# Kernel optimization log

Measured on AMD Instinct MI355X. Metric: run time of the kernel, lower is better.

The kernel has to match this reference:

```python
import jax, jax.numpy as jnp
import numpy as np

N_NODES = 100000
NEG_SLOPE = 0.01


def setup_inputs() -> dict:
    key = jax.random.key(0)
    k1, k2, k3, k4 = jax.random.split(key, 4)
    E = 1600000
    x = jax.random.normal(k1, (N_NODES, 256), dtype=jnp.float32)
    edge_index = jax.random.randint(k2, (2, E), 0, N_NODES, dtype=jnp.int64)
    # Glorot-ish init for GCN linear weights
    W1 = jax.random.normal(k3, (256, 128), dtype=jnp.float32) / np.sqrt(256.0)
    b1 = jnp.zeros((128,), dtype=jnp.float32)
    W2 = jax.random.normal(k4, (128, 64), dtype=jnp.float32) / np.sqrt(128.0)
    b2 = jnp.zeros((64,), dtype=jnp.float32)
    return {"x": x, "edge_index": edge_index, "W1": W1, "b1": b1, "W2": W2, "b2": b2}


def _gcn_norm(edge_index, n_nodes):
    # Add self-loops (PyG GCNConv default), symmetric normalization.
    loops = jnp.arange(n_nodes, dtype=edge_index.dtype)
    src = jnp.concatenate([edge_index[0], loops])
    dst = jnp.concatenate([edge_index[1], loops])
    deg = jax.ops.segment_sum(jnp.ones_like(dst, dtype=jnp.float32), dst,
                              num_segments=n_nodes)
    dinv = jnp.where(deg > 0, 1.0 / jnp.sqrt(deg), 0.0)
    norm = dinv[src] * dinv[dst]  # [E + N]
    return src, dst, norm


def _gcn_conv(h, W, b, src, dst, norm, n_nodes):
    h = h @ W                              # [N, out] linear transform first
    msg = h[src] * norm[:, None]           # gather + edge weighting
    agg = jax.ops.segment_sum(msg, dst, num_segments=n_nodes)  # scatter-add
    return agg + b


def reference(x, edge_index, W1, b1, W2, b2):
    n = x.shape[0]
    src, dst, norm = _gcn_norm(edge_index, n)
    h = _gcn_conv(x, W1, b1, src, dst, norm, n)
    h = jnp.where(h >= 0, h, NEG_SLOPE * h)  # leaky_relu, slope 0.01
    return _gcn_conv(h, W2, b2, src, dst, norm, n)
```

## Files before the change

### kernel.cpp

```cpp
#include <hip/hip_runtime.h>
#include <hip/hip_bf16.h>
#include <stdint.h>

#define GPART 512
#define BSHIFT 9
#define BSIZE 512
#define MAXNB 512

typedef short short8 __attribute__((ext_vector_type(8)));
typedef float f32x4 __attribute__((ext_vector_type(4)));
union U4S8 { uint4 u; short8 s; };

static __device__ __forceinline__ float bflo(uint32_t h){ return __uint_as_float(h << 16); }
static __device__ __forceinline__ float bfhi(uint32_t h){ return __uint_as_float(h & 0xFFFF0000u); }
static __device__ __forceinline__ uint32_t f2bf_bits(float f){
  uint32_t u = __float_as_uint(f);
  return (u + 0x7FFFu + ((u >> 16) & 1u)) >> 16;
}
static __device__ __forceinline__ uint32_t pack2bf(float lo, float hi){
  return f2bf_bits(lo) | (f2bf_bits(hi) << 16);
}

__global__ __launch_bounds__(256) void k_hist(const int* __restrict__ dst, int E, int NB,
    int* __restrict__ gHist){
  __shared__ int lh[MAXNB];
  int blk = blockIdx.x;
  for (int i = threadIdx.x; i < NB; i += 256) lh[i] = 0;
  __syncthreads();
  int chunk = (E + GPART - 1) / GPART;
  int e0 = blk * chunk, e1 = min(E, e0 + chunk);
  for (int e = e0 + threadIdx.x; e < e1; e += 256)
    atomicAdd(&lh[dst[e] >> BSHIFT], 1);
  __syncthreads();
  for (int i = threadIdx.x; i < NB; i += 256) gHist[i * GPART + blk] = lh[i];
}

__global__ __launch_bounds__(64) void k_scanA(int* __restrict__ gHist,
    int* __restrict__ bucketTotal){
  int b = blockIdx.x;
  int lane = threadIdx.x;
  int carry = 0;
  #pragma unroll
  for (int r = 0; r < GPART/64; ++r){
    int v = gHist[b*GPART + r*64 + lane];
    int pref = v;
    #pragma unroll
    for (int off = 1; off < 64; off <<= 1){ int t = __shfl_up(pref, off); if (lane >= off) pref += t; }
    int tot = __shfl(pref, 63);
    gHist[b*GPART + r*64 + lane] = carry + pref - v;
    carry += tot;
  }
  if (lane == 0) bucketTotal[b] = carry;
}

__global__ __launch_bounds__(64) void k_scanB(const int* __restrict__ bucketTotal, int NB,
    int* __restrict__ bucketBase){
  int lane = threadIdx.x;
  int carry = 0;
  for (int r = 0; r*64 < NB; ++r){
    int idx = r*64 + lane;
    int v = (idx < NB) ? bucketTotal[idx] : 0;
    int pref = v;
    #pragma unroll
    for (int off = 1; off < 64; off <<= 1){ int t = __shfl_up(pref, off); if (lane >= off) pref += t; }
    int tot = __shfl(pref, 63);
    if (idx < NB) bucketBase[idx] = carry + pref - v;
    carry += tot;
  }
}

__global__ __launch_bounds__(256) void k_scatter(const int* __restrict__ src,
    const int* __restrict__ dst, int E, int NB,
    const int* __restrict__ gHist, const int* __restrict__ bucketBase,
    uint32_t* __restrict__ edgesP){
  __shared__ int lpos[MAXNB];
  int blk = blockIdx.x;
  for (int i = threadIdx.x; i < NB; i += 256) lpos[i] = 0;
  __syncthreads();
  int chunk = (E + GPART - 1) / GPART;
  int e0 = blk * chunk, e1 = min(E, e0 + chunk);
  for (int e = e0 + threadIdx.x; e < e1; e += 256){
    int s = src[e], d = dst[e];
    int b = d >> BSHIFT;
    int o = atomicAdd(&lpos[b], 1);
    int pos = bucketBase[b] + gHist[b*GPART + blk] + o;
    edgesP[pos] = (uint32_t)s | ((uint32_t)(d & (BSIZE-1)) << 23);
  }
}

__global__ __launch_bounds__(256) void k_buildcsr(const uint32_t* __restrict__ edgesP,
    const int* __restrict__ bucketBase, const int* __restrict__ bucketTotal,
    int n, int* __restrict__ start, int* __restrict__ cnt, float* __restrict__ dinv,
    int* __restrict__ csr){
  __shared__ int cnt_l[BSIZE], start_l[BSIZE], fp[BSIZE];
  int b = blockIdx.x;
  int base = bucketBase[b], total = bucketTotal[b];
  int d0 = b << BSHIFT;
  int tid = threadIdx.x;
  for (int i = tid; i < BSIZE; i += 256){ cnt_l[i] = 0; fp[i] = 0; }
  __syncthreads();
  for (int i = tid; i < total; i += 256)
    atomicAdd(&cnt_l[edgesP[base + i] >> 23], 1);
  __syncthreads();
  if (tid < 64){
    int lane = tid, carry = 0;
    #pragma unroll
    for (int r = 0; r < BSIZE/64; ++r){
      int v = cnt_l[r*64 + lane];
      int pref = v;
      #pragma unroll
      for (int off = 1; off < 64; off <<= 1){ int t = __shfl_up(pref, off); if (lane >= off) pref += t; }
      int tot = __shfl(pref, 63);
      start_l[r*64 + lane] = carry + pref - v;
      carry += tot;
    }
  }
  __syncthreads();
  for (int i = tid; i < BSIZE; i += 256){
    int d = d0 + i;
    if (d < n){
      int c = cnt_l[i];
      cnt[d] = c;
      start[d] = base + start_l[i];
      dinv[d] = rsqrtf((float)(c + 1));
    }
  }
  for (int i = tid; i < total; i += 256){
    uint32_t w = edgesP[base + i];
    int dl = (int)(w >> 23);
    int s = (int)(w & 0x7FFFFFu);
    int p = atomicAdd(&fp[dl], 1);
    csr[base + start_l[dl] + p] = s;
  }
}

__global__ __launch_bounds__(256) void k_packW(const float* __restrict__ W,
    uint4* __restrict__ Wf, int K, int Nc){
  int s = blockIdx.x * 256 + threadIdx.x;
  int total = (K >> 5) * (Nc >> 4) * 64;
  if (s >= total) return;
  int lane = s & 63;
  int frag = s >> 6;
  int NT = Nc >> 4;
  int nt = frag % NT, ks = frag / NT;
  int col = nt*16 + (lane & 15);
  int k0  = ks*32 + (lane >> 4)*8;
  float v[8];
  #pragma unroll
  for (int e = 0; e < 8; ++e) v[e] = W[(size_t)(k0 + e)*Nc + col];
  uint4 u;
  u.x = pack2bf(v[0], v[1]); u.y = pack2bf(v[2], v[3]);
  u.z = pack2bf(v[4], v[5]); u.w = pack2bf(v[6], v[7]);
  Wf[s] = u;
}

__global__ __launch_bounds__(256) void k_gemm1_mfma(const float* __restrict__ X,
    const uint4* __restrict__ W1f, unsigned short* __restrict__ H1, int n){
  int wv = (int)((blockIdx.x * 256u + threadIdx.x) >> 6);
  int lane = threadIdx.x & 63;
  int row0 = wv * 16;
  if (row0 >= n) return;
  int rA = lane & 15, kg = lane >> 4;
  f32x4 acc[8];
  #pragma unroll
  for (int nt = 0; nt < 8; ++nt) acc[nt] = (f32x4){0.f, 0.f, 0.f, 0.f};
  int r0 = min(row0 + rA, n - 1);
  const float* x0 = X + (size_t)r0*256 + kg*8;
  float4 fa = *(const float4*)(x0);
  float4 fb = *(const float4*)(x0 + 4);
  for (int ks = 0; ks < 8; ++ks){
    U4S8 a;
    a.u.x = pack2bf(fa.x, fa.y); a.u.y = pack2bf(fa.z, fa.w);
    a.u.z = pack2bf(fb.x, fb.y); a.u.w = pack2bf(fb.z, fb.w);
    if (ks < 7){
      fa = *(const float4*)(x0 + (ks+1)*32);
      fb = *(const float4*)(x0 + (ks+1)*32 + 4);
    }
    #pragma unroll
    for (int nt = 0; nt < 8; ++nt){
      U4S8 b; b.u = W1f[(ks*8 + nt)*64 + lane];
      acc[nt] = __builtin_amdgcn_mfma_f32_16x16x32_bf16(a.s, b.s, acc[nt], 0, 0, 0);
    }
  }
  #pragma unroll
  for (int r = 0; r < 4; ++r){
    int row = row0 + kg*4 + r;
    if (row < n){
      #pragma unroll
      for (int nt = 0; nt < 8; ++nt)
        H1[(size_t)row*128 + nt*16 + rA] = (unsigned short)f2bf_bits(acc[nt][r]);
    }
  }
}

__global__ __launch_bounds__(256) void k_agg1(const uint32_t* __restrict__ H1,
    const int* __restrict__ csr,
    const int* __restrict__ start, const int* __restrict__ cnt,
    const float* __restrict__ dinv, const float* __restrict__ b1,
    uint32_t* __restrict__ A1, int n){
  int w = (int)((blockIdx.x * blockDim.x + threadIdx.x) >> 6);
  int lane = threadIdx.x & 63;
  if (w >= n) return;
  float dw = dinv[w];
  uint32_t h = H1[(size_t)w*64 + lane];
  float sw = dw * dw;
  float a0 = sw * bflo(h), a1 = sw * bfhi(h);
  int e0 = start[w], deg = cnt[w];
  for (int base = 0; base < deg; base += 64){
    int nin = min(64, deg - base);
    int sE = (lane < nin) ? csr[e0 + base + lane] : 0;
    float dvE = (lane < nin) ? dinv[sE] : 0.f;
    for (int j = 0; j < nin; j += 8){
      int ss[8]; float wts[8];
      #pragma unroll
      for (int u = 0; u < 8; ++u){
        int jj = j + u;
        int s = __shfl(sE, jj & 63);
        float dv = __shfl(dvE, jj & 63);
        bool ok = jj < nin;
        ss[u] = ok ? s : w;
        wts[u] = ok ? dv * dw : 0.f;
      }
      uint32_t hh[8];
      #pragma unroll
      for (int u = 0; u < 8; ++u) hh[u] = H1[(size_t)ss[u]*64 + lane];
      #pragma unroll
      for (int u = 0; u < 8; ++u){
        a0 = fmaf(wts[u], bflo(hh[u]), a0);
        a1 = fmaf(wts[u], bfhi(hh[u]), a1);
      }
    }
  }
  a0 += b1[lane*2]; a1 += b1[lane*2+1];
  a0 = (a0 >= 0.f) ? a0 : 0.01f * a0;
  a1 = (a1 >= 0.f) ? a1 : 0.01f * a1;
  A1[(size_t)w*64 + lane] = pack2bf(a0, a1);
}

__global__ __launch_bounds__(256) void k_gemm2_mfma(const uint4* __restrict__ A1,
    const uint4* __restrict__ W2f, unsigned short* __restrict__ H2, int n){
  int wv = (int)((blockIdx.x * 256u + threadIdx.x) >> 6);
  int lane = threadIdx.x & 63;
  int row0 = wv * 16;
  if (row0 >= n) return;
  int rA = lane & 15, kg = lane >> 4;
  f32x4 acc[4];
  #pragma unroll
  for (int nt = 0; nt < 4; ++nt) acc[nt] = (f32x4){0.f, 0.f, 0.f, 0.f};
  int r0 = min(row0 + rA, n - 1);
  const uint4* arow = A1 + (size_t)r0*16 + kg;
  uint4 u = arow[0];
  #pragma unroll
  for (int ks = 0; ks < 4; ++ks){
    U4S8 a; a.u = u;
    if (ks < 3) u = arow[(ks+1)*4];
    #pragma unroll
    for (int nt = 0; nt < 4; ++nt){
      U4S8 b; b.u = W2f[(ks*4 + nt)*64 + lane];
      acc[nt] = __builtin_amdgcn_mfma_f32_16x16x32_bf16(a.s, b.s, acc[nt], 0, 0, 0);
    }
  }
  #pragma unroll
  for (int r = 0; r < 4; ++r){
    int row = row0 + kg*4 + r;
    if (row < n){
      #pragma unroll
      for (int nt = 0; nt < 4; ++nt)
        H2[(size_t)row*64 + nt*16 + rA] = (unsigned short)f2bf_bits(acc[nt][r]);
    }
  }
}

__global__ __launch_bounds__(256) void k_agg2(const unsigned short* __restrict__ H2,
    const int* __restrict__ csr,
    const int* __restrict__ start, const int* __restrict__ cnt,
    const float* __restrict__ dinv, const float* __restrict__ b2,
    float* __restrict__ out, int n){
  int w = (int)((blockIdx.x * blockDim.x + threadIdx.x) >> 6);
  int lane = threadIdx.x & 63;
  if (w >= n) return;
  float dw = dinv[w];
  float a = dw * dw * __uint_as_float(((uint32_t)H2[(size_t)w*64 + lane]) << 16);
  int e0 = start[w], deg = cnt[w];
  for (int base = 0; base < deg; base += 64){
    int nin = min(64, deg - base);
    int sE = (lane < nin) ? csr[e0 + base + lane] : 0;
    float dvE = (lane < nin) ? dinv[sE] : 0.f;
    for (int j = 0; j < nin; j += 8){
      int ss[8]; float wts[8];
      #pragma unroll
      for (int u = 0; u < 8; ++u){
        int jj = j + u;
        int s = __shfl(sE, jj & 63);
        float dv = __shfl(dvE, jj & 63);
        bool ok = jj < nin;
        ss[u] = ok ? s : w;
        wts[u] = ok ? dv * dw : 0.f;
      }
      unsigned short hh[8];
      #pragma unroll
      for (int u = 0; u < 8; ++u) hh[u] = H2[(size_t)ss[u]*64 + lane];
      #pragma unroll
      for (int u = 0; u < 8; ++u)
        a = fmaf(wts[u], __uint_as_float(((uint32_t)hh[u]) << 16), a);
    }
  }
  out[(size_t)w*64 + lane] = a + b2[lane];
}

extern "C" void kernel_launch(void* const* d_in, const int* in_sizes, int n_in,
                              void* d_out, int out_size, void* d_ws, size_t ws_size,
                              hipStream_t stream){
  const float* x  = (const float*)d_in[0];
  const int*   ei = (const int*)d_in[1];
  const float* W1 = (const float*)d_in[2];
  const float* b1 = (const float*)d_in[3];
  const float* W2 = (const float*)d_in[4];
  const float* b2 = (const float*)d_in[5];
  float* out = (float*)d_out;

  int N = in_sizes[0] / 256;
  int E = in_sizes[1] / 2;
  int NB = (N + BSIZE - 1) >> BSHIFT;

  char* p = (char*)d_ws;
  uint32_t* H1   = (uint32_t*)p;  p += (size_t)N*64*4;
  uint32_t* A1   = (uint32_t*)p;  p += (size_t)N*64*4;
  uint32_t* H2   = (uint32_t*)p;  p += (size_t)N*32*4;
  uint32_t* edgesP=(uint32_t*)p;  p += (size_t)E*4;
  int* csr       = (int*)p;       p += (size_t)E*4;
  int* gHist     = (int*)p;       p += (size_t)NB*GPART*4;
  int* bucketTotal=(int*)p;       p += (size_t)((NB+63)&~63)*4;
  int* bucketBase= (int*)p;       p += (size_t)((NB+63)&~63)*4;
  uint4* W1f     = (uint4*)p;     p += 8*8*64*16;
  uint4* W2f     = (uint4*)p;     p += 4*4*64*16;
  int* start     = (int*)p;       p += (size_t)N*4;
  int* cnt       = (int*)p;       p += (size_t)N*4;
  float* dinv    = (float*)p;     p += (size_t)N*4;

  const int* srcIdx = ei;
  const int* dstIdx = ei + E;

  int nW = (N + 15) / 16;
  int nWaveBlocks = (nW + 3) / 4;

  k_packW<<<(8*8*64 + 255)/256, 256, 0, stream>>>(W1, W1f, 256, 128);
  k_packW<<<(4*4*64 + 255)/256, 256, 0, stream>>>(W2, W2f, 128, 64);
  k_hist<<<GPART, 256, 0, stream>>>(dstIdx, E, NB, gHist);
  k_scanA<<<NB, 64, 0, stream>>>(gHist, bucketTotal);
  k_scanB<<<1, 64, 0, stream>>>(bucketTotal, NB, bucketBase);
  k_scatter<<<GPART, 256, 0, stream>>>(srcIdx, dstIdx, E, NB, gHist, bucketBase, edgesP);
  k_buildcsr<<<NB, 256, 0, stream>>>(edgesP, bucketBase, bucketTotal, N, start, cnt, dinv, csr);
  k_gemm1_mfma<<<nWaveBlocks, 256, 0, stream>>>(x, W1f, (unsigned short*)H1, N);
  k_agg1<<<(N+3)/4, 256, 0, stream>>>(H1, csr, start, cnt, dinv, b1, A1, N);
  k_gemm2_mfma<<<nWaveBlocks, 256, 0, stream>>>((const uint4*)A1, W2f, (unsigned short*)H2, N);
  k_agg2<<<(N+3)/4, 256, 0, stream>>>((const unsigned short*)H2, csr, start, cnt, dinv, b2, out, N);
}
```

Baseline: 214.0 us.

## Precompute edge weights into CSR and vectorize aggregation gathers across edge groups

CSR construction is split into two kernels, so the second can store each neighbour index together with its precomputed normalization weight as an int2. This removes the dependent dinv[src] gather from both aggregation kernels. The aggregation kernels now read feature rows as 16-byte vectors, with sub-groups of the wave handling different edges at once, then combine partial sums with cross-lane xor shuffles. The cost is twice the CSR storage and traffic, one extra kernel launch, and a shuffle reduction at the end of each aggregation.

```diff
diff --git a/kernel.cpp b/kernel.cpp
--- a/kernel.cpp
+++ b/kernel.cpp
@@ -88,16 +88,15 @@
   }
 }
 
-__global__ __launch_bounds__(256) void k_buildcsr(const uint32_t* __restrict__ edgesP,
+__global__ __launch_bounds__(256) void k_csr_p1(const uint32_t* __restrict__ edgesP,
     const int* __restrict__ bucketBase, const int* __restrict__ bucketTotal,
-    int n, int* __restrict__ start, int* __restrict__ cnt, float* __restrict__ dinv,
-    int* __restrict__ csr){
-  __shared__ int cnt_l[BSIZE], start_l[BSIZE], fp[BSIZE];
+    int n, int* __restrict__ start, int* __restrict__ cnt, float* __restrict__ dinv){
+  __shared__ int cnt_l[BSIZE], start_l[BSIZE];
   int b = blockIdx.x;
   int base = bucketBase[b], total = bucketTotal[b];
   int d0 = b << BSHIFT;
   int tid = threadIdx.x;
-  for (int i = tid; i < BSIZE; i += 256){ cnt_l[i] = 0; fp[i] = 0; }
+  for (int i = tid; i < BSIZE; i += 256) cnt_l[i] = 0;
   __syncthreads();
   for (int i = tid; i < total; i += 256)
     atomicAdd(&cnt_l[edgesP[base + i] >> 23], 1);
@@ -125,12 +124,26 @@
       dinv[d] = rsqrtf((float)(c + 1));
     }
   }
+}
+
+__global__ __launch_bounds__(256) void k_csr_p2(const uint32_t* __restrict__ edgesP,
+    const int* __restrict__ bucketBase, const int* __restrict__ bucketTotal,
+    const int* __restrict__ start, const float* __restrict__ dinv,
+    int2* __restrict__ csr){
+  __shared__ int fp[BSIZE];
+  int b = blockIdx.x;
+  int base = bucketBase[b], total = bucketTotal[b];
+  int d0 = b << BSHIFT;
+  int tid = threadIdx.x;
+  for (int i = tid; i < BSIZE; i += 256) fp[i] = 0;
+  __syncthreads();
   for (int i = tid; i < total; i += 256){
     uint32_t w = edgesP[base + i];
     int dl = (int)(w >> 23);
     int s = (int)(w & 0x7FFFFFu);
     int p = atomicAdd(&fp[dl], 1);
-    csr[base + start_l[dl] + p] = s;
+    float wt = dinv[s] * dinv[d0 + dl];
+    csr[start[d0 + dl] + p] = make_int2(s, __float_as_int(wt));
   }
 }
 
@@ -193,48 +206,59 @@
   }
 }
 
-__global__ __launch_bounds__(256) void k_agg1(const uint32_t* __restrict__ H1,
-    const int* __restrict__ csr,
+__global__ __launch_bounds__(256) void k_agg1(const uint4* __restrict__ H1,
+    const int2* __restrict__ csr,
     const int* __restrict__ start, const int* __restrict__ cnt,
     const float* __restrict__ dinv, const float* __restrict__ b1,
-    uint32_t* __restrict__ A1, int n){
+    uint4* __restrict__ A1, int n){
   int w = (int)((blockIdx.x * blockDim.x + threadIdx.x) >> 6);
   int lane = threadIdx.x & 63;
   if (w >= n) return;
+  int g = lane >> 4, li = lane & 15;
   float dw = dinv[w];
-  uint32_t h = H1[(size_t)w*64 + lane];
-  float sw = dw * dw;
-  float a0 = sw * bflo(h), a1 = sw * bfhi(h);
+  float sw = (g == 0) ? dw * dw : 0.f;
+  uint4 hs = H1[(size_t)w*16 + li];
+  float acc[8];
+  acc[0]=sw*bflo(hs.x); acc[1]=sw*bfhi(hs.x); acc[2]=sw*bflo(hs.y); acc[3]=sw*bfhi(hs.y);
+  acc[4]=sw*bflo(hs.z); acc[5]=sw*bfhi(hs.z); acc[6]=sw*bflo(hs.w); acc[7]=sw*bfhi(hs.w);
   int e0 = start[w], deg = cnt[w];
   for (int base = 0; base < deg; base += 64){
     int nin = min(64, deg - base);
-    int sE = (lane < nin) ? csr[e0 + base + lane] : 0;
-    float dvE = (lane < nin) ? dinv[sE] : 0.f;
+    int2 ew = (lane < nin) ? csr[e0 + base + lane] : make_int2(0, 0);
     for (int j = 0; j < nin; j += 8){
-      int ss[8]; float wts[8];
-      #pragma unroll
-      for (int u = 0; u < 8; ++u){
-        int jj = j + u;
-        int s = __shfl(sE, jj & 63);
-        float dv = __shfl(dvE, jj & 63);
-        bool ok = jj < nin;
-        ss[u] = ok ? s : w;
-        wts[u] = ok ? dv * dw : 0.f;
-      }
-      uint32_t hh[8];
-      #pragma unroll
-      for (int u = 0; u < 8; ++u) hh[u] = H1[(size_t)ss[u]*64 + lane];
-      #pragma unroll
-      for (int u = 0; u < 8; ++u){
-        a0 = fmaf(wts[u], bflo(hh[u]), a0);
-        a1 = fmaf(wts[u], bfhi(hh[u]), a1);
-      }
-    }
-  }
-  a0 += b1[lane*2]; a1 += b1[lane*2+1];
-  a0 = (a0 >= 0.f) ? a0 : 0.01f * a0;
-  a1 = (a1 >= 0.f) ? a1 : 0.01f * a1;
-  A1[(size_t)w*64 + lane] = pack2bf(a0, a1);
+      int   sA = __shfl(ew.x, j + g);
+      float wA = __uint_as_float((uint32_t)__shfl(ew.y, j + g));
+      int   sB = __shfl(ew.x, j + 4 + g);
+      float wB = __uint_as_float((uint32_t)__shfl(ew.y, j + 4 + g));
+      uint4 hA = H1[(size_t)sA*16 + li];
+      uint4 hB = H1[(size_t)sB*16 + li];
+      acc[0]=fmaf(wA,bflo(hA.x),acc[0]); acc[1]=fmaf(wA,bfhi(hA.x),acc[1]);
+      acc[2]=fmaf(wA,bflo(hA.y),acc[2]); acc[3]=fmaf(wA,bfhi(hA.y),acc[3]);
+      acc[4]=fmaf(wA,bflo(hA.z),acc[4]); acc[5]=fmaf(wA,bfhi(hA.z),acc[5]);
+      acc[6]=fmaf(wA,bflo(hA.w),acc[6]); acc[7]=fmaf(wA,bfhi(hA.w),acc[7]);
+      acc[0]=fmaf(wB,bflo(hB.x),acc[0]); acc[1]=fmaf(wB,bfhi(hB.x),acc[1]);
+      acc[2]=fmaf(wB,bflo(hB.y),acc[2]); acc[3]=fmaf(wB,bfhi(hB.y),acc[3]);
+      acc[4]=fmaf(wB,bflo(hB.z),acc[4]); acc[5]=fmaf(wB,bfhi(hB.z),acc[5]);
+      acc[6]=fmaf(wB,bflo(hB.w),acc[6]); acc[7]=fmaf(wB,bfhi(hB.w),acc[7]);
+    }
+  }
+  #pragma unroll
+  for (int e = 0; e < 8; ++e){
+    acc[e] += __shfl_xor(acc[e], 16);
+    acc[e] += __shfl_xor(acc[e], 32);
+  }
+  float4 bA = *(const float4*)&b1[li*8];
+  float4 bB = *(const float4*)&b1[li*8 + 4];
+  acc[0]+=bA.x; acc[1]+=bA.y; acc[2]+=bA.z; acc[3]+=bA.w;
+  acc[4]+=bB.x; acc[5]+=bB.y; acc[6]+=bB.z; acc[7]+=bB.w;
+  #pragma unroll
+  for (int e = 0; e < 8; ++e) acc[e] = (acc[e] >= 0.f) ? acc[e] : 0.01f * acc[e];
+  if (g == 0){
+    uint4 o;
+    o.x = pack2bf(acc[0], acc[1]); o.y = pack2bf(acc[2], acc[3]);
+    o.z = pack2bf(acc[4], acc[5]); o.w = pack2bf(acc[6], acc[7]);
+    A1[(size_t)w*16 + li] = o;
+  }
 }
 
 __global__ __launch_bounds__(256) void k_gemm2_mfma(const uint4* __restrict__ A1,
@@ -271,41 +295,58 @@
   }
 }
 
-__global__ __launch_bounds__(256) void k_agg2(const unsigned short* __restrict__ H2,
-    const int* __restrict__ csr,
+__global__ __launch_bounds__(256) void k_agg2(const uint4* __restrict__ H2,
+    const int2* __restrict__ csr,
     const int* __restrict__ start, const int* __restrict__ cnt,
     const float* __restrict__ dinv, const float* __restrict__ b2,
     float* __restrict__ out, int n){
   int w = (int)((blockIdx.x * blockDim.x + threadIdx.x) >> 6);
   int lane = threadIdx.x & 63;
   if (w >= n) return;
+  int g = lane >> 3, li = lane & 7;
   float dw = dinv[w];
-  float a = dw * dw * __uint_as_float(((uint32_t)H2[(size_t)w*64 + lane]) << 16);
+  float sw = (g == 0) ? dw * dw : 0.f;
+  uint4 hs = H2[(size_t)w*8 + li];
+  float acc[8];
+  acc[0]=sw*bflo(hs.x); acc[1]=sw*bfhi(hs.x); acc[2]=sw*bflo(hs.y); acc[3]=sw*bfhi(hs.y);
+  acc[4]=sw*bflo(hs.z); acc[5]=sw*bfhi(hs.z); acc[6]=sw*bflo(hs.w); acc[7]=sw*bfhi(hs.w);
   int e0 = start[w], deg = cnt[w];
   for (int base = 0; base < deg; base += 64){
     int nin = min(64, deg - base);
-    int sE = (lane < nin) ? csr[e0 + base + lane] : 0;
-    float dvE = (lane < nin) ? dinv[sE] : 0.f;
-    for (int j = 0; j < nin; j += 8){
-      int ss[8]; float wts[8];
-      #pragma unroll
-      for (int u = 0; u < 8; ++u){
-        int jj = j + u;
-        int s = __shfl(sE, jj & 63);
-        float dv = __shfl(dvE, jj & 63);
-        bool ok = jj < nin;
-        ss[u] = ok ? s : w;
-        wts[u] = ok ? dv * dw : 0.f;
-      }
-      unsigned short hh[8];
-      #pragma unroll
-      for (int u = 0; u < 8; ++u) hh[u] = H2[(size_t)ss[u]*64 + lane];
-      #pragma unroll
-      for (int u = 0; u < 8; ++u)
-        a = fmaf(wts[u], __uint_as_float(((uint32_t)hh[u]) << 16), a);
-    }
-  }
-  out[(size_t)w*64 + lane] = a + b2[lane];
+    int2 ew = (lane < nin) ? csr[e0 + base + lane] : make_int2(0, 0);
+    for (int j = 0; j < nin; j += 16){
+      int   sA = __shfl(ew.x, j + g);
+      float wA = __uint_as_float((uint32_t)__shfl(ew.y, j + g));
+      int   sB = __shfl(ew.x, j + 8 + g);
+      float wB = __uint_as_float((uint32_t)__shfl(ew.y, j + 8 + g));
+      uint4 hA = H2[(size_t)sA*8 + li];
+      uint4 hB = H2[(size_t)sB*8 + li];
+      acc[0]=fmaf(wA,bflo(hA.x),acc[0]); acc[1]=fmaf(wA,bfhi(hA.x),acc[1]);
+      acc[2]=fmaf(wA,bflo(hA.y),acc[2]); acc[3]=fmaf(wA,bfhi(hA.y),acc[3]);
+      acc[4]=fmaf(wA,bflo(hA.z),acc[4]); acc[5]=fmaf(wA,bfhi(hA.z),acc[5]);
+      acc[6]=fmaf(wA,bflo(hA.w),acc[6]); acc[7]=fmaf(wA,bfhi(hA.w),acc[7]);
+      acc[0]=fmaf(wB,bflo(hB.x),acc[0]); acc[1]=fmaf(wB,bfhi(hB.x),acc[1]);
+      acc[2]=fmaf(wB,bflo(hB.y),acc[2]); acc[3]=fmaf(wB,bfhi(hB.y),acc[3]);
+      acc[4]=fmaf(wB,bflo(hB.z),acc[4]); acc[5]=fmaf(wB,bfhi(hB.z),acc[5]);
+      acc[6]=fmaf(wB,bflo(hB.w),acc[6]); acc[7]=fmaf(wB,bfhi(hB.w),acc[7]);
+    }
+  }
+  #pragma unroll
+  for (int e = 0; e < 8; ++e){
+    acc[e] += __shfl_xor(acc[e], 8);
+    acc[e] += __shfl_xor(acc[e], 16);
+    acc[e] += __shfl_xor(acc[e], 32);
+  }
+  float4 bA = *(const float4*)&b2[li*8];
+  float4 bB = *(const float4*)&b2[li*8 + 4];
+  acc[0]+=bA.x; acc[1]+=bA.y; acc[2]+=bA.z; acc[3]+=bA.w;
+  acc[4]+=bB.x; acc[5]+=bB.y; acc[6]+=bB.z; acc[7]+=bB.w;
+  if (g == 0){
+    float4 o0 = make_float4(acc[0], acc[1], acc[2], acc[3]);
+    float4 o1 = make_float4(acc[4], acc[5], acc[6], acc[7]);
+    *(float4*)&out[(size_t)w*64 + li*8]     = o0;
+    *(float4*)&out[(size_t)w*64 + li*8 + 4] = o1;
+  }
 }
 
 extern "C" void kernel_launch(void* const* d_in, const int* in_sizes, int n_in,
@@ -328,7 +369,7 @@
   uint32_t* A1   = (uint32_t*)p;  p += (size_t)N*64*4;
   uint32_t* H2   = (uint32_t*)p;  p += (size_t)N*32*4;
   uint32_t* edgesP=(uint32_t*)p;  p += (size_t)E*4;
-  int* csr       = (int*)p;       p += (size_t)E*4;
+  int2* csr      = (int2*)p;      p += (size_t)E*8;
   int* gHist     = (int*)p;       p += (size_t)NB*GPART*4;
   int* bucketTotal=(int*)p;       p += (size_t)((NB+63)&~63)*4;
   int* bucketBase= (int*)p;       p += (size_t)((NB+63)&~63)*4;
@@ -350,9 +391,10 @@
   k_scanA<<<NB, 64, 0, stream>>>(gHist, bucketTotal);
   k_scanB<<<1, 64, 0, stream>>>(bucketTotal, NB, bucketBase);
   k_scatter<<<GPART, 256, 0, stream>>>(srcIdx, dstIdx, E, NB, gHist, bucketBase, edgesP);
-  k_buildcsr<<<NB, 256, 0, stream>>>(edgesP, bucketBase, bucketTotal, N, start, cnt, dinv, csr);
+  k_csr_p1<<<NB, 256, 0, stream>>>(edgesP, bucketBase, bucketTotal, N, start, cnt, dinv);
+  k_csr_p2<<<NB, 256, 0, stream>>>(edgesP, bucketBase, bucketTotal, start, dinv, csr);
   k_gemm1_mfma<<<nWaveBlocks, 256, 0, stream>>>(x, W1f, (unsigned short*)H1, N);
-  k_agg1<<<(N+3)/4, 256, 0, stream>>>(H1, csr, start, cnt, dinv, b1, A1, N);
+  k_agg1<<<(N+3)/4, 256, 0, stream>>>((const uint4*)H1, csr, start, cnt, dinv, b1, (uint4*)A1, N);
   k_gemm2_mfma<<<nWaveBlocks, 256, 0, stream>>>((const uint4*)A1, W2f, (unsigned short*)H2, N);
-  k_agg2<<<(N+3)/4, 256, 0, stream>>>((const unsigned short*)H2, csr, start, cnt, dinv, b2, out, N);
-}
+  k_agg2<<<(N+3)/4, 256, 0, stream>>>((const uint4*)H2, csr, start, cnt, dinv, b2, out, N);
+}
```

New measurement: 216.4 us. About the same (+1.1%).
